# Kernel tuning notes

Hardware: AMD Instinct MI355X
Metric: run time of the kernel (lower is better)

Reference implementation:

```python
import jax, jax.numpy as jnp
import numpy as np

ALPHA = 0.2  # LeakyReLU negative slope


def setup_inputs() -> dict:
    key = jax.random.key(0)
    k1, k2, k3, k4 = jax.random.split(key, 4)
    B, N, F_IN, F_OUT = 8, 2048, 512, 256
    h = jax.random.normal(k1, (B, N, F_IN), dtype=jnp.float32)
    # torch nn.Linear weights: [out, in]
    W = jax.random.normal(k2, (F_OUT, F_IN), dtype=jnp.float32) * (1.414 / np.sqrt(F_IN))
    a1 = jax.random.normal(k3, (1, F_OUT), dtype=jnp.float32) * (1.414 / np.sqrt(F_OUT))
    a2 = jax.random.normal(k4, (1, F_OUT), dtype=jnp.float32) * (1.414 / np.sqrt(F_OUT))
    return {"h": h, "W": W, "a1": a1, "a2": a2}


def reference(h, W, a1, a2):
    # Wh: [B, N, F_out]
    Wh = jnp.einsum('bnf,of->bno', h, W)
    # additive attention scores
    s1 = jnp.einsum('bno,o->bn', Wh, a1[0])  # [B, N]
    s2 = jnp.einsum('bno,o->bn', Wh, a2[0])  # [B, N]
    e = s1[:, :, None] + s2[:, None, :]       # [B, N, N]
    e = jnp.where(e > 0, e, ALPHA * e)         # LeakyReLU
    attention = jax.nn.softmax(e, axis=2)      # softmax over last dim
    # dropout p=0.0 -> identity
    h_prime = jnp.einsum('bnm,bmo->bno', attention, Wh)
    return jax.nn.elu(h_prime)  # concat=True path
```

## Files before the change

### kernel.cpp

```cpp
#include <hip/hip_runtime.h>

typedef __attribute__((ext_vector_type(8))) _Float16 half8;
typedef __attribute__((ext_vector_type(4))) _Float16 half4;
typedef __attribute__((ext_vector_type(4))) float f32x4;
#if __has_builtin(__builtin_amdgcn_cvt_pkrtz)
typedef __attribute__((ext_vector_type(2))) __fp16 fp16x2;
#endif

#define ALPHA 0.2f
#define LOG2E 1.44269504f

__device__ __forceinline__ void gload_lds16(const void* g, void* l) {
  __builtin_amdgcn_global_load_lds((const __attribute__((address_space(1))) unsigned int*)g,
                                   (__attribute__((address_space(3))) unsigned int*)l, 16, 0, 0);
}

__device__ __forceinline__ float fexp2(float x) {
#if __has_builtin(__builtin_amdgcn_exp2f)
  return __builtin_amdgcn_exp2f(x);
#else
  return exp2f(x);
#endif
}

#if __has_builtin(__builtin_amdgcn_cvt_pkrtz)
#define PACK2(DST, I, A, B)                        \
  { fp16x2 q_ = __builtin_amdgcn_cvt_pkrtz(A, B);  \
    DST[I] = (_Float16)q_[0]; DST[I + 1] = (_Float16)q_[1]; }
#else
#define PACK2(DST, I, A, B) { DST[I] = (_Float16)(A); DST[I + 1] = (_Float16)(B); }
#endif

#define EXP8(OUT, V0, V1, C1_, C2_)                                   \
  {                                                                   \
    float p0 = fexp2(fmaxf(C1_ + V0.x, fmaf(ALPHA, V0.x, C2_)));      \
    float p1 = fexp2(fmaxf(C1_ + V0.y, fmaf(ALPHA, V0.y, C2_)));      \
    float p2 = fexp2(fmaxf(C1_ + V0.z, fmaf(ALPHA, V0.z, C2_)));      \
    float p3 = fexp2(fmaxf(C1_ + V0.w, fmaf(ALPHA, V0.w, C2_)));      \
    float p4 = fexp2(fmaxf(C1_ + V1.x, fmaf(ALPHA, V1.x, C2_)));      \
    float p5 = fexp2(fmaxf(C1_ + V1.y, fmaf(ALPHA, V1.y, C2_)));      \
    float p6 = fexp2(fmaxf(C1_ + V1.z, fmaf(ALPHA, V1.z, C2_)));      \
    float p7 = fexp2(fmaxf(C1_ + V1.w, fmaf(ALPHA, V1.w, C2_)));      \
    PACK2(OUT, 0, p0, p1); PACK2(OUT, 2, p2, p3);                     \
    PACK2(OUT, 4, p4, p5); PACK2(OUT, 6, p6, p7);                     \
  }

__global__ __launch_bounds__(256) void k_prologue(const float* __restrict__ W,
                                                  const float* __restrict__ a1,
                                                  const float* __restrict__ a2,
                                                  _Float16* __restrict__ W16,
                                                  float* __restrict__ u1,
                                                  float* __restrict__ u2) {
  const int bid = blockIdx.x, t = threadIdx.x;
  if (bid < 128) {
    int idx4 = bid * 256 + t;
    int n = idx4 >> 7;
    int q = idx4 & 127;
    float4 v = *reinterpret_cast<const float4*>(W + n * 512 + q * 4);
    half4 hv = {(_Float16)v.x, (_Float16)v.y, (_Float16)v.z, (_Float16)v.w};
    int kp = (q * 4) ^ ((n & 7) << 3);
    *reinterpret_cast<half4*>(W16 + n * 512 + kp) = hv;
  } else {
    __shared__ float p1[4][64], p2[4][64];
    int l = t & 63, g = t >> 6;
    int k = (bid - 128) * 64 + l;
    float x1 = 0.f, x2 = 0.f;
    for (int o = g * 64; o < g * 64 + 64; ++o) {
      float wv = W[o * 512 + k];
      x1 += wv * a1[o];
      x2 += wv * a2[o];
    }
    p1[g][l] = x1; p2[g][l] = x2;
    __syncthreads();
    if (g == 0) {
      u1[k] = p1[0][l] + p1[1][l] + p1[2][l] + p1[3][l];
      u2[k] = p2[0][l] + p2[1][l] + p2[2][l] + p2[3][l];
    }
  }
}

__global__ __launch_bounds__(256) void k_gemm_wh(const float* __restrict__ h,
                                                 const _Float16* __restrict__ W16,
                                                 const float* __restrict__ u1,
                                                 const float* __restrict__ u2,
                                                 float* __restrict__ s1o,
                                                 float* __restrict__ s2o,
                                                 _Float16* __restrict__ WhT) {
  __shared__ _Float16 Ab[2][32 * 64];
  __shared__ _Float16 Bb[2][256 * 64];
  const int t = threadIdx.x, lane = t & 63, w = t >> 6;
  const int i0 = blockIdx.x * 32;
  const int b = i0 >> 11, n0 = i0 & 2047;
  const int ar = t >> 3, au = t & 7;
  const float* hrow = h + (size_t)(i0 + ar) * 512 + au * 8;

  f32x4 acc[2][4];
#pragma unroll
  for (int mi = 0; mi < 2; ++mi)
#pragma unroll
    for (int ni = 0; ni < 4; ++ni) acc[mi][ni] = (f32x4){0.f, 0.f, 0.f, 0.f};

  float4 aR0 = *reinterpret_cast<const float4*>(hrow);
  float4 aR1 = *reinterpret_cast<const float4*>(hrow + 4);
#pragma unroll
  for (int q = 0; q < 8; ++q) {
    int idx = (q * 4 + w) * 64 + lane;
    int nn = idx >> 3, uu = idx & 7;
    gload_lds16(W16 + nn * 512 + uu * 8, (char*)&Bb[0][0] + idx * 16);
  }
  float x1 = 0.f, x2 = 0.f;

  for (int kt = 0; kt < 8; ++kt) {
    const int cur = kt & 1;
    {
      half8 av;
      av[0] = (_Float16)aR0.x; av[1] = (_Float16)aR0.y;
      av[2] = (_Float16)aR0.z; av[3] = (_Float16)aR0.w;
      av[4] = (_Float16)aR1.x; av[5] = (_Float16)aR1.y;
      av[6] = (_Float16)aR1.z; av[7] = (_Float16)aR1.w;
      *reinterpret_cast<half8*>((char*)&Ab[cur][0] + ar * 128 + ((au * 16) ^ ((ar & 7) << 4))) = av;
      const float* up1 = u1 + kt * 64 + au * 8;
      const float* up2 = u2 + kt * 64 + au * 8;
      float4 u1a = *reinterpret_cast<const float4*>(up1);
      float4 u1b = *reinterpret_cast<const float4*>(up1 + 4);
      float4 u2a = *reinterpret_cast<const float4*>(up2);
      float4 u2b = *reinterpret_cast<const float4*>(up2 + 4);
      x1 += aR0.x * u1a.x + aR0.y * u1a.y + aR0.z * u1a.z + aR0.w * u1a.w
          + aR1.x * u1b.x + aR1.y * u1b.y + aR1.z * u1b.z + aR1.w * u1b.w;
      x2 += aR0.x * u2a.x + aR0.y * u2a.y + aR0.z * u2a.z + aR0.w * u2a.w
          + aR1.x * u2b.x + aR1.y * u2b.y + aR1.z * u2b.z + aR1.w * u2b.w;
    }
    __syncthreads();
    if (kt < 7) {
      const int k0 = (kt + 1) * 64;
      aR0 = *reinterpret_cast<const float4*>(hrow + k0);
      aR1 = *reinterpret_cast<const float4*>(hrow + k0 + 4);
#pragma unroll
      for (int q = 0; q < 8; ++q) {
        int idx = (q * 4 + w) * 64 + lane;
        int nn = idx >> 3, uu = idx & 7;
        gload_lds16(W16 + nn * 512 + k0 + uu * 8, (char*)&Bb[cur ^ 1][0] + idx * 16);
      }
    }
    const char* Ac = (const char*)&Ab[cur][0];
    const char* Bc = (const char*)&Bb[cur][0];
#pragma unroll
    for (int kk = 0; kk < 2; ++kk) {
      const int jb = (lane >> 4) * 16 + kk * 64;
      half8 afr[2];
#pragma unroll
      for (int mi = 0; mi < 2; ++mi) {
        int rr = (lane & 15) + 16 * mi;
        afr[mi] = *reinterpret_cast<const half8*>(Ac + rr * 128 + (jb ^ ((rr & 7) << 4)));
      }
#pragma unroll
      for (int ni = 0; ni < 4; ++ni) {
        int nn = 64 * w + 16 * ni + (lane & 15);
        half8 bfr = *reinterpret_cast<const half8*>(Bc + nn * 128 + (jb ^ ((nn & 7) << 4)));
#pragma unroll
        for (int mi = 0; mi < 2; ++mi)
          acc[mi][ni] = __builtin_amdgcn_mfma_f32_16x16x32_f16(afr[mi], bfr, acc[mi][ni], 0, 0, 0);
      }
    }
  }
  x1 += __shfl_xor(x1, 1); x1 += __shfl_xor(x1, 2); x1 += __shfl_xor(x1, 4);
  x2 += __shfl_xor(x2, 1); x2 += __shfl_xor(x2, 2); x2 += __shfl_xor(x2, 4);
  if (au == 0) { s1o[i0 + ar] = x1; s2o[i0 + ar] = x2; }
  _Float16* whtb = WhT + (size_t)b * 256 * 2048;
#pragma unroll
  for (int mi = 0; mi < 2; ++mi)
#pragma unroll
    for (int ni = 0; ni < 4; ++ni) {
      int c = 64 * w + 16 * ni + (lane & 15);
      int nb = n0 + 16 * mi + (lane >> 4) * 4;
      int np = nb ^ ((c & 7) << 3);
      f32x4 a = acc[mi][ni];
      half4 hv = {(_Float16)a[0], (_Float16)a[1], (_Float16)a[2], (_Float16)a[3]};
      *reinterpret_cast<half4*>(whtb + (size_t)c * 2048 + np) = hv;
    }
}

__global__ __launch_bounds__(512) void k_attn(const _Float16* __restrict__ WhT,
                                              const float* __restrict__ s1,
                                              const float* __restrict__ s2,
                                              float* __restrict__ out) {
  __shared__ _Float16 Bb[3][128 * 64];
  __shared__ _Float16 Pb[2][64 * 64];
  __shared__ float s2s[2048];
  __shared__ float red[8];
  __shared__ float d_lds[64];
  const int t = threadIdx.x, lane = t & 63, w = t >> 6;
  const int rg = w >> 1, cg = w & 1;
  const int b = blockIdx.x & 7;
  const int i0 = ((blockIdx.x >> 3) & 31) * 64;
  const int ch = blockIdx.x >> 8;
  const _Float16* whtb = WhT + ((size_t)b * 256 + ch * 128) * 2048;
  const int arow = lane & 15;
  const int pr = t >> 3, pj8 = t & 7;
  const float s1v = s1[b * 2048 + i0 + pr];

  float4 sv4 = *reinterpret_cast<const float4*>(s2 + b * 2048 + t * 4);
  float m0 = fmaxf(fmaxf(sv4.x, sv4.y), fmaxf(sv4.z, sv4.w));
  *reinterpret_cast<float4*>(&s2s[t * 4]) =
      make_float4(sv4.x * LOG2E, sv4.y * LOG2E, sv4.z * LOG2E, sv4.w * LOG2E);
#pragma unroll
  for (int off = 32; off >= 1; off >>= 1) m0 = fmaxf(m0, __shfl_xor(m0, off));
  if (lane == 0) red[w] = m0;
  __syncthreads();
  float smaxL;
  {
    float mm = fmaxf(fmaxf(red[0], red[1]), fmaxf(red[2], red[3]));
    mm = fmaxf(mm, fmaxf(fmaxf(red[4], red[5]), fmaxf(red[6], red[7])));
    smaxL = mm * LOG2E;
  }
  const float s1L = LOG2E * s1v;
  const float e0L = s1L + smaxL;
  const float mrowL = fmaxf(e0L, ALPHA * e0L);
  const float C1 = s1L - mrowL;
  const float C2 = fmaf(ALPHA, s1L, -mrowL);
  const int pwoff = pr * 128 + ((pj8 * 16) ^ ((pr & 7) << 4));
  half8 onesb;
  {
    _Float16 ov = (arow == 0) ? (_Float16)1.0f : (_Float16)0.0f;
#pragma unroll
    for (int x = 0; x < 8; ++x) onesb[x] = ov;
  }
  f32x4 acc[4];
#pragma unroll
  for (int ni = 0; ni < 4; ++ni) acc[ni] = (f32x4){0.f, 0.f, 0.f, 0.f};
  f32x4 accd = (f32x4){0.f, 0.f, 0.f, 0.f};

  {
    const float* sp = &s2s[pj8 * 8];
    float4 v0 = *reinterpret_cast<const float4*>(sp);
    float4 v1 = *reinterpret_cast<const float4*>(sp + 4);
    half8 ph;
    EXP8(ph, v0, v1, C1, C2);
    *reinterpret_cast<half8*>((char*)&Pb[0][0] + pwoff) = ph;
  }
#pragma unroll
  for (int x = 0; x < 2; ++x)
#pragma unroll
    for (int q = 0; q < 2; ++q) {
      int idx = q * 512 + t;
      int cl = idx >> 3, uu = idx & 7;
      gload_lds16(whtb + (size_t)cl * 2048 + x * 64 + uu * 8, (char*)&Bb[x][0] + idx * 16);
    }

  for (int jt = 0; jt < 32; ++jt) {
    if (jt < 31) asm volatile("s_waitcnt vmcnt(2) lgkmcnt(0)" ::: "memory");
    else         asm volatile("s_waitcnt vmcnt(0) lgkmcnt(0)" ::: "memory");
    __builtin_amdgcn_s_barrier();
    if (jt < 30) {
      const int j0n = (jt + 2) * 64;
      const int p = (jt + 2) % 3;
#pragma unroll
      for (int q = 0; q < 2; ++q) {
        int idx = q * 512 + t;
        int cl = idx >> 3, uu = idx & 7;
        gload_lds16(whtb + (size_t)cl * 2048 + j0n + uu * 8, (char*)&Bb[p][0] + idx * 16);
      }
    }
    if (jt < 31) {
      const float* sp = &s2s[(jt + 1) * 64 + pj8 * 8];
      float4 v0 = *reinterpret_cast<const float4*>(sp);
      float4 v1 = *reinterpret_cast<const float4*>(sp + 4);
      half8 ph;
      EXP8(ph, v0, v1, C1, C2);
      *reinterpret_cast<half8*>((char*)&Pb[(jt + 1) & 1][0] + pwoff) = ph;
    }
    const char* Bc = (const char*)&Bb[jt % 3][0];
    const char* Pc = (const char*)&Pb[jt & 1][0];
#pragma unroll
    for (int kk = 0; kk < 2; ++kk) {
      const int jb = ((lane >> 4) * 8 + kk * 32) * 2;
      const int ar64 = rg * 16 + arow;
      half8 afr = *reinterpret_cast<const half8*>(Pc + ar64 * 128 + (jb ^ ((ar64 & 7) << 4)));
      if (cg == 0)
        accd = __builtin_amdgcn_mfma_f32_16x16x32_f16(afr, onesb, accd, 0, 0, 0);
#pragma unroll
      for (int ni = 0; ni < 4; ++ni) {
        int cl = cg * 64 + 16 * ni + arow;
        half8 bfr = *reinterpret_cast<const half8*>(Bc + cl * 128 + (jb ^ ((cl & 7) << 4)));
        acc[ni] = __builtin_amdgcn_mfma_f32_16x16x32_f16(afr, bfr, acc[ni], 0, 0, 0);
      }
    }
  }
  if (cg == 0 && arow == 0) {
#pragma unroll
    for (int reg = 0; reg < 4; ++reg)
      d_lds[rg * 16 + (lane >> 4) * 4 + reg] = accd[reg];
  }
  __syncthreads();
  const size_t ob = ((size_t)b * 2048 + i0 + rg * 16) * 256 + ch * 128 + cg * 64;
#pragma unroll
  for (int reg = 0; reg < 4; ++reg) {
    int rr = (lane >> 4) * 4 + reg;
    float inv = 1.0f / d_lds[rg * 16 + rr];
#pragma unroll
    for (int ni = 0; ni < 4; ++ni) {
      int c = 16 * ni + arow;
      float v = acc[ni][reg] * inv;
      v = v > 0.f ? v : (__expf(v) - 1.f);
      out[ob + (size_t)rr * 256 + c] = v;
    }
  }
}

extern "C" void kernel_launch(void* const* d_in, const int* in_sizes, int n_in,
                              void* d_out, int out_size, void* d_ws, size_t ws_size,
                              hipStream_t stream) {
  (void)in_sizes; (void)n_in; (void)out_size; (void)ws_size;
  const float* h = (const float*)d_in[0];
  const float* W = (const float*)d_in[1];
  const float* a1 = (const float*)d_in[2];
  const float* a2 = (const float*)d_in[3];
  float* out = (float*)d_out;
  char* ws = (char*)d_ws;
  _Float16* WhT = (_Float16*)(ws);
  _Float16* W16 = (_Float16*)(ws + 8388608);
  float* u1 = (float*)(ws + 8650752);
  float* u2 = (float*)(ws + 8652800);
  float* s1 = (float*)(ws + 8654848);
  float* s2 = (float*)(ws + 8720384);

  hipLaunchKernelGGL(k_prologue, dim3(136), dim3(256), 0, stream, W, a1, a2, W16, u1, u2);
  hipLaunchKernelGGL(k_gemm_wh, dim3(512), dim3(256), 0, stream, h, W16, u1, u2, s1, s2, WhT);
  hipLaunchKernelGGL(k_attn, dim3(512), dim3(512), 0, stream, WhT, s1, s2, out);
}
```

Baseline: 67.07 us.

## Replace quadratic attention with sorted prefix-sum formulation of LeakyReLU softmax

Because the score is s1_i + s2_j passed through a piecewise-linear LeakyReLU, each exp term factors into a row part times a column part, with the branch set by whether s2_j exceeds -s1_i. The new path sorts s2 per batch and builds prefix sums of exp(s2)·Wh and exp(αs2)·Wh. Each output row then becomes a binary search plus a few vector combinations, replacing the O(N²·F) attention matmul with O(N·F) work. The trade-off is several extra small launches, a serial bitonic sort and scans, large fp32 prefix buffers, and possible numerical error from unshifted exponentials and prefix-sum subtraction. It is used only when the workspace is large enough; otherwise the old kernel runs.

```diff
diff --git a/kernel.cpp b/kernel.cpp
--- a/kernel.cpp
+++ b/kernel.cpp
@@ -9,6 +9,7 @@
 
 #define ALPHA 0.2f
 #define LOG2E 1.44269504f
+#define ALC (ALPHA * LOG2E)
 
 __device__ __forceinline__ void gload_lds16(const void* g, void* l) {
   __builtin_amdgcn_global_load_lds((const __attribute__((address_space(1))) unsigned int*)g,
@@ -85,7 +86,8 @@
                                                  const float* __restrict__ u2,
                                                  float* __restrict__ s1o,
                                                  float* __restrict__ s2o,
-                                                 _Float16* __restrict__ WhT) {
+                                                 _Float16* __restrict__ WhOut,
+                                                 const int mode) {
   __shared__ _Float16 Ab[2][32 * 64];
   __shared__ _Float16 Bb[2][256 * 64];
   const int t = threadIdx.x, lane = t & 63, w = t >> 6;
@@ -166,24 +168,218 @@
   x1 += __shfl_xor(x1, 1); x1 += __shfl_xor(x1, 2); x1 += __shfl_xor(x1, 4);
   x2 += __shfl_xor(x2, 1); x2 += __shfl_xor(x2, 2); x2 += __shfl_xor(x2, 4);
   if (au == 0) { s1o[i0 + ar] = x1; s2o[i0 + ar] = x2; }
-  _Float16* whtb = WhT + (size_t)b * 256 * 2048;
-#pragma unroll
-  for (int mi = 0; mi < 2; ++mi)
-#pragma unroll
-    for (int ni = 0; ni < 4; ++ni) {
-      int c = 64 * w + 16 * ni + (lane & 15);
-      int nb = n0 + 16 * mi + (lane >> 4) * 4;
-      int np = nb ^ ((c & 7) << 3);
-      f32x4 a = acc[mi][ni];
-      half4 hv = {(_Float16)a[0], (_Float16)a[1], (_Float16)a[2], (_Float16)a[3]};
-      *reinterpret_cast<half4*>(whtb + (size_t)c * 2048 + np) = hv;
-    }
-}
-
-__global__ __launch_bounds__(512) void k_attn(const _Float16* __restrict__ WhT,
-                                              const float* __restrict__ s1,
-                                              const float* __restrict__ s2,
-                                              float* __restrict__ out) {
+  if (mode) {
+#pragma unroll
+    for (int mi = 0; mi < 2; ++mi)
+#pragma unroll
+      for (int ni = 0; ni < 4; ++ni) {
+        int c = 64 * w + 16 * ni + (lane & 15);
+        int g = i0 + 16 * mi + (lane >> 4) * 4;
+        f32x4 a = acc[mi][ni];
+#pragma unroll
+        for (int reg = 0; reg < 4; ++reg)
+          WhOut[(size_t)(g + reg) * 256 + c] = (_Float16)a[reg];
+      }
+  } else {
+    _Float16* whtb = WhOut + (size_t)b * 256 * 2048;
+#pragma unroll
+    for (int mi = 0; mi < 2; ++mi)
+#pragma unroll
+      for (int ni = 0; ni < 4; ++ni) {
+        int c = 64 * w + 16 * ni + (lane & 15);
+        int nb = n0 + 16 * mi + (lane >> 4) * 4;
+        int np = nb ^ ((c & 7) << 3);
+        f32x4 a = acc[mi][ni];
+        half4 hv = {(_Float16)a[0], (_Float16)a[1], (_Float16)a[2], (_Float16)a[3]};
+        *reinterpret_cast<half4*>(whtb + (size_t)c * 2048 + np) = hv;
+      }
+  }
+}
+
+__global__ __launch_bounds__(512) void k_sort(const float* __restrict__ s2,
+                                              float* __restrict__ tS,
+                                              int* __restrict__ perm) {
+  __shared__ float key[2048];
+  __shared__ int idx[2048];
+  const int b = blockIdx.x, t = threadIdx.x;
+  for (int i = t; i < 2048; i += 512) { key[i] = s2[b * 2048 + i]; idx[i] = i; }
+  __syncthreads();
+  for (int k = 2; k <= 2048; k <<= 1) {
+    for (int j = k >> 1; j > 0; j >>= 1) {
+      for (int i = t; i < 2048; i += 512) {
+        int ixj = i ^ j;
+        if (ixj > i) {
+          bool asc = ((i & k) == 0);
+          float ka = key[i], kb = key[ixj];
+          bool sw = asc ? (ka > kb) : (ka < kb);
+          if (sw) {
+            key[i] = kb; key[ixj] = ka;
+            int tmp = idx[i]; idx[i] = idx[ixj]; idx[ixj] = tmp;
+          }
+        }
+      }
+      __syncthreads();
+    }
+  }
+  for (int i = t; i < 2048; i += 512) { tS[b * 2048 + i] = key[i]; perm[b * 2048 + i] = idx[i]; }
+}
+
+__global__ __launch_bounds__(256) void k_csum(const _Float16* __restrict__ Wh16,
+                                              const float* __restrict__ tS,
+                                              const int* __restrict__ perm,
+                                              float* __restrict__ Cp,
+                                              float* __restrict__ Cn) {
+  const int bid = blockIdx.x;
+  const int b = bid >> 6, ch = bid & 63, t = threadIdx.x;
+  const int base = b * 2048 + ch * 32;
+  float rp = 0.f, rn = 0.f;
+  for (int r = 0; r < 32; ++r) {
+    int row = perm[base + r];
+    float tv = tS[base + r];
+    float wp = fexp2(LOG2E * tv);
+    float wn = fexp2(ALC * tv);
+    float v = (float)Wh16[((size_t)b * 2048 + row) * 256 + t];
+    rp = fmaf(wp, v, rp);
+    rn = fmaf(wn, v, rn);
+  }
+  Cp[(size_t)bid * 256 + t] = rp;
+  Cn[(size_t)bid * 256 + t] = rn;
+}
+
+__global__ __launch_bounds__(256) void k_cscan(float* __restrict__ Cp, float* __restrict__ Cn) {
+  const int b = blockIdx.x, c = threadIdx.x;
+  float ap = 0.f, an = 0.f;
+  for (int ch = 0; ch < 64; ++ch) {
+    size_t o = ((size_t)(b * 64 + ch)) * 256 + c;
+    float vp = Cp[o], vn = Cn[o];
+    Cp[o] = ap; Cn[o] = an;
+    ap += vp; an += vn;
+  }
+}
+
+__global__ __launch_bounds__(256) void k_sscan(const float* __restrict__ tS,
+                                               float* __restrict__ pp,
+                                               float* __restrict__ pn) {
+  __shared__ float sp[256], sn[256];
+  const int b = blockIdx.x, t = threadIdx.x;
+  float lp[8], ln[8];
+  float ap = 0.f, an = 0.f;
+#pragma unroll
+  for (int x = 0; x < 8; ++x) {
+    float tv = tS[b * 2048 + t * 8 + x];
+    lp[x] = ap; ln[x] = an;
+    ap += fexp2(LOG2E * tv);
+    an += fexp2(ALC * tv);
+  }
+  sp[t] = ap; sn[t] = an;
+  __syncthreads();
+  if (t == 0) {
+    float s = 0.f, s2_ = 0.f;
+    for (int i = 0; i < 256; ++i) {
+      float v = sp[i]; sp[i] = s; s += v;
+      float v2 = sn[i]; sn[i] = s2_; s2_ += v2;
+    }
+  }
+  __syncthreads();
+  float bp = sp[t], bn = sn[t];
+#pragma unroll
+  for (int x = 0; x < 8; ++x) {
+    pp[b * 2049 + t * 8 + x] = bp + lp[x];
+    pn[b * 2049 + t * 8 + x] = bn + ln[x];
+  }
+  if (t == 255) {
+    pp[b * 2049 + 2048] = bp + ap;
+    pn[b * 2049 + 2048] = bn + an;
+  }
+}
+
+__global__ __launch_bounds__(256) void k_fg(const _Float16* __restrict__ Wh16,
+                                            const float* __restrict__ tS,
+                                            const int* __restrict__ perm,
+                                            const float* __restrict__ Cp,
+                                            const float* __restrict__ Cn,
+                                            float* __restrict__ Pp,
+                                            float* __restrict__ Pn) {
+  const int bid = blockIdx.x;
+  const int b = bid >> 6, ch = bid & 63, t = threadIdx.x;
+  const int base = b * 2048 + ch * 32;
+  float rp = Cp[(size_t)bid * 256 + t];
+  float rn = Cn[(size_t)bid * 256 + t];
+  for (int r = 0; r < 32; ++r) {
+    int k = ch * 32 + r;
+    size_t po = ((size_t)b * 2049 + k) * 256 + t;
+    Pp[po] = rp; Pn[po] = rn;
+    int row = perm[base + r];
+    float tv = tS[base + r];
+    float wp = fexp2(LOG2E * tv);
+    float wn = fexp2(ALC * tv);
+    float v = (float)Wh16[((size_t)b * 2048 + row) * 256 + t];
+    rp = fmaf(wp, v, rp);
+    rn = fmaf(wn, v, rn);
+  }
+  if (ch == 63) {
+    size_t po = ((size_t)b * 2049 + 2048) * 256 + t;
+    Pp[po] = rp; Pn[po] = rn;
+  }
+}
+
+__global__ __launch_bounds__(256) void k_out(const float* __restrict__ s1,
+                                             const float* __restrict__ tS,
+                                             const float* __restrict__ pp,
+                                             const float* __restrict__ pn,
+                                             const float* __restrict__ Pp,
+                                             const float* __restrict__ Pn,
+                                             float* __restrict__ out) {
+  __shared__ float tSh[2048];
+  __shared__ float pps[2049], pns[2049];
+  const int bid = blockIdx.x;
+  const int b = bid & 7, grp = bid >> 3;
+  const int t = threadIdx.x;
+  for (int i = t; i < 2048; i += 256) tSh[i] = tS[b * 2048 + i];
+  for (int i = t; i < 2049; i += 256) { pps[i] = pp[b * 2049 + i]; pns[i] = pn[b * 2049 + i]; }
+  __syncthreads();
+  const int rl = t >> 3, q = t & 7;
+  const int i = grp * 32 + rl;
+  const float s1v = s1[b * 2048 + i];
+  const float tmax = tSh[2047];
+  const float e0 = s1v + tmax;
+  const float m = fmaxf(e0, ALPHA * e0);
+  const float A = fexp2(LOG2E * (s1v - m));
+  const float B = fexp2(LOG2E * fmaf(ALPHA, s1v, -m));
+  const float thr = -s1v;
+  int k = 0;
+#pragma unroll
+  for (int s = 2048; s >= 1; s >>= 1) {
+    int nk = k + s;
+    if (nk <= 2048 && tSh[nk - 1] <= thr) k = nk;
+  }
+  const float d = B * pns[k] + A * (pps[2048] - pps[k]);
+  const float inv = 1.0f / d;
+  const float4* fp4 = (const float4*)(Pp + ((size_t)b * 2049 + k) * 256);
+  const float4* fn4 = (const float4*)(Pn + ((size_t)b * 2049 + k) * 256);
+  const float4* tt4 = (const float4*)(Pp + ((size_t)b * 2049 + 2048) * 256);
+  float4* op = (float4*)(out + ((size_t)b * 2048 + i) * 256);
+#pragma unroll
+  for (int x = 0; x < 8; ++x) {
+    int c4 = x * 8 + q;
+    float4 fp = fp4[c4], fn = fn4[c4], tt = tt4[c4];
+    float4 v;
+    v.x = (B * fn.x + A * (tt.x - fp.x)) * inv;
+    v.y = (B * fn.y + A * (tt.y - fp.y)) * inv;
+    v.z = (B * fn.z + A * (tt.z - fp.z)) * inv;
+    v.w = (B * fn.w + A * (tt.w - fp.w)) * inv;
+    v.x = v.x > 0.f ? v.x : (__expf(v.x) - 1.f);
+    v.y = v.y > 0.f ? v.y : (__expf(v.y) - 1.f);
+    v.z = v.z > 0.f ? v.z : (__expf(v.z) - 1.f);
+    v.w = v.w > 0.f ? v.w : (__expf(v.w) - 1.f);
+    op[c4] = v;
+  }
+}
+
+__global__ __launch_bounds__(512) void k_attn_fb(const _Float16* __restrict__ WhT,
+                                                 const float* __restrict__ s1,
+                                                 const float* __restrict__ s2,
+                                                 float* __restrict__ out) {
   __shared__ _Float16 Bb[3][128 * 64];
   __shared__ _Float16 Pb[2][64 * 64];
   __shared__ float s2s[2048];
@@ -229,7 +425,6 @@
 #pragma unroll
   for (int ni = 0; ni < 4; ++ni) acc[ni] = (f32x4){0.f, 0.f, 0.f, 0.f};
   f32x4 accd = (f32x4){0.f, 0.f, 0.f, 0.f};
-
   {
     const float* sp = &s2s[pj8 * 8];
     float4 v0 = *reinterpret_cast<const float4*>(sp);
@@ -246,7 +441,6 @@
       int cl = idx >> 3, uu = idx & 7;
       gload_lds16(whtb + (size_t)cl * 2048 + x * 64 + uu * 8, (char*)&Bb[x][0] + idx * 16);
     }
-
   for (int jt = 0; jt < 32; ++jt) {
     if (jt < 31) asm volatile("s_waitcnt vmcnt(2) lgkmcnt(0)" ::: "memory");
     else         asm volatile("s_waitcnt vmcnt(0) lgkmcnt(0)" ::: "memory");
@@ -310,21 +504,40 @@
 extern "C" void kernel_launch(void* const* d_in, const int* in_sizes, int n_in,
                               void* d_out, int out_size, void* d_ws, size_t ws_size,
                               hipStream_t stream) {
-  (void)in_sizes; (void)n_in; (void)out_size; (void)ws_size;
+  (void)in_sizes; (void)n_in; (void)out_size;
   const float* h = (const float*)d_in[0];
   const float* W = (const float*)d_in[1];
   const float* a1 = (const float*)d_in[2];
   const float* a2 = (const float*)d_in[3];
   float* out = (float*)d_out;
   char* ws = (char*)d_ws;
-  _Float16* WhT = (_Float16*)(ws);
+  _Float16* Wh16 = (_Float16*)(ws);
   _Float16* W16 = (_Float16*)(ws + 8388608);
   float* u1 = (float*)(ws + 8650752);
   float* u2 = (float*)(ws + 8652800);
   float* s1 = (float*)(ws + 8654848);
   float* s2 = (float*)(ws + 8720384);
+  float* tS = (float*)(ws + 8785920);
+  int* perm = (int*)(ws + 8851456);
+  float* pp = (float*)(ws + 8916992);
+  float* pn = (float*)(ws + 8982560);
+  float* Cp = (float*)(ws + 9048128);
+  float* Cn = (float*)(ws + 9572416);
+  float* Pp = (float*)(ws + 10096704);
+  float* Pn = (float*)(ws + 26882112);
+  const bool big = (ws_size >= (size_t)43667520);
 
   hipLaunchKernelGGL(k_prologue, dim3(136), dim3(256), 0, stream, W, a1, a2, W16, u1, u2);
-  hipLaunchKernelGGL(k_gemm_wh, dim3(512), dim3(256), 0, stream, h, W16, u1, u2, s1, s2, WhT);
-  hipLaunchKernelGGL(k_attn, dim3(512), dim3(512), 0, stream, WhT, s1, s2, out);
-}
+  hipLaunchKernelGGL(k_gemm_wh, dim3(512), dim3(256), 0, stream, h, W16, u1, u2, s1, s2,
+                     Wh16, big ? 1 : 0);
+  if (big) {
+    hipLaunchKernelGGL(k_sort, dim3(8), dim3(512), 0, stream, s2, tS, perm);
+    hipLaunchKernelGGL(k_csum, dim3(512), dim3(256), 0, stream, Wh16, tS, perm, Cp, Cn);
+    hipLaunchKernelGGL(k_cscan, dim3(8), dim3(256), 0, stream, Cp, Cn);
+    hipLaunchKernelGGL(k_sscan, dim3(8), dim3(256), 0, stream, tS, pp, pn);
+    hipLaunchKernelGGL(k_fg, dim3(512), dim3(256), 0, stream, Wh16, tS, perm, Cp, Cn, Pp, Pn);
+    hipLaunchKernelGGL(k_out, dim3(512), dim3(256), 0, stream, s1, tS, pp, pn, Pp, Pn, out);
+  } else {
+    hipLaunchKernelGGL(k_attn_fb, dim3(512), dim3(512), 0, stream, Wh16, s1, s2, out);
+  }
+}
```

Result: slower. 118.8 us (+77.2%).
